# Kernel tuning notes

Hardware: AMD Instinct MI355X
Metric: run time of the kernel (lower is better)

## Reference

```python
import jax, jax.numpy as jnp
import numpy as np

N = 50000
E = 500000
D = 128      # input_nf = output_nf = hidden_nf
EPS = 1e-8
MAX_TRANS = 10.0


def setup_inputs() -> dict:
    key = jax.random.key(0)
    ks = jax.random.split(key, 16)
    s = lambda k, shp: jax.random.normal(k, shp, dtype=jnp.float32) * 0.05
    inp = {
        "h": jax.random.normal(ks[0], (N, D), dtype=jnp.float32),
        "edge_index": jax.random.randint(ks[1], (2, E), 0, N, dtype=jnp.int64),
        "coord": jax.random.normal(ks[2], (N, 3), dtype=jnp.float32),
        # edge_mlp: Linear(2D+1 -> D), SiLU, Linear(D -> D), SiLU
        "We1": s(ks[3], (2 * D + 1, D)), "be1": jnp.zeros((D,), jnp.float32),
        "We2": s(ks[4], (D, D)),         "be2": jnp.zeros((D,), jnp.float32),
        # att_mlp: Linear(D -> 1), Sigmoid
        "Watt": s(ks[5], (D, 1)), "batt": jnp.zeros((1,), jnp.float32),
        # coord_mlp: Linear(D -> D), SiLU, Linear(D -> 1, bias=False, xavier gain=0.001)
        "Wc1": s(ks[6], (D, D)), "bc1": jnp.zeros((D,), jnp.float32),
        "Wc2": s(ks[7], (D, 1)) * 0.001,
        # node_mlp: Linear(2D -> D), SiLU, Linear(D -> D)
        "Wn1": s(ks[8], (2 * D, D)), "bn1": jnp.zeros((D,), jnp.float32),
        "Wn2": s(ks[9], (D, D)),     "bn2": jnp.zeros((D,), jnp.float32),
    }
    return inp


def _segment_mean(data, seg_ids, num_segments):
    tot = jax.ops.segment_sum(data, seg_ids, num_segments=num_segments)
    cnt = jax.ops.segment_sum(jnp.ones_like(data), seg_ids, num_segments=num_segments)
    return tot / jnp.clip(cnt, 1.0, None)


def reference(h, edge_index, coord, We1, be1, We2, be2, Watt, batt,
              Wc1, bc1, Wc2, Wn1, bn1, Wn2, bn2):
    row, col = edge_index[0], edge_index[1]

    # coord2radial (normalize=False)
    coord_diff = coord[row] - coord[col]                      # [E, 3]
    radial = jnp.sum(coord_diff ** 2, axis=1, keepdims=True)  # [E, 1]

    # edge_model with attention
    e_in = jnp.concatenate([h[row], h[col], radial], axis=1)  # [E, 2D+1]
    e = jax.nn.silu(e_in @ We1 + be1)
    edge_feat = jax.nn.silu(e @ We2 + be2)                    # [E, D]
    att = jax.nn.sigmoid(edge_feat @ Watt + batt)             # [E, 1]
    edge_feat = edge_feat * att

    # coord_model (update_coords=True, coords_agg='mean', tanh=False)
    cw = jax.nn.silu(edge_feat @ Wc1 + bc1) @ Wc2             # [E, 1]
    trans = jnp.clip(coord_diff * cw, -MAX_TRANS, MAX_TRANS)  # [E, 3]
    agg_c = jnp.clip(_segment_mean(trans, row, N), -MAX_TRANS, MAX_TRANS)
    coord_out = coord + agg_c

    # node_model (residual=True)
    agg = jax.ops.segment_sum(edge_feat, row, num_segments=N)  # [N, D]
    n_in = jnp.concatenate([h, agg], axis=1)                   # [N, 2D]
    h_out = h + (jax.nn.silu(n_in @ Wn1 + bn1) @ Wn2 + bn2)

    return h_out, coord_out, edge_feat
```

## Files before the change

kernel.cpp:

```cpp
#include <hip/hip_runtime.h>

typedef unsigned short ushort_t;
typedef __attribute__((ext_vector_type(8))) short short8;
typedef __attribute__((ext_vector_type(4))) short short4v;
typedef __attribute__((ext_vector_type(4))) float f32x4;

#define NN 50000
#define EE 500000
#define DD 128
#define MAXT 10.0f

#define MFMA(a,b,c) __builtin_amdgcn_mfma_f32_16x16x32_bf16((a),(b),(c),0,0,0)

__device__ __forceinline__ ushort_t f2bf(float x){
  unsigned u = __float_as_uint(x);
  u += 0x7FFFu + ((u>>16)&1u);
  return (ushort_t)(u>>16);
}
__device__ __forceinline__ float sigm(float x){ return 1.0f/(1.0f+__expf(-x)); }
__device__ __forceinline__ float siluf(float x){ return x*sigm(x); }
__device__ __forceinline__ float clamp10(float x){ return fminf(fmaxf(x,-MAXT),MAXT); }

__global__ void k_prep(const float* __restrict__ We1, const float* __restrict__ We2,
                       const float* __restrict__ Wc1, const float* __restrict__ Wn1,
                       const float* __restrict__ Wn2, ushort_t* __restrict__ wpre)
{
  int idx = blockIdx.x*256 + threadIdx.x;
  if (idx >= 7*16384) return;
  int mat = idx >> 14;
  int loc = idx & 16383;
  int n = loc >> 7;
  int kidx = loc & 127;
  int ko = 16*(kidx&7) + (kidx>>3);
  float v;
  switch(mat){
    case 0: v = We1[kidx*DD + n]; break;
    case 1: v = We1[(128+kidx)*DD + n]; break;
    case 2: v = We2[kidx*DD + n]; break;
    case 3: v = Wc1[ko*DD + n]; break;
    case 4: v = Wn1[kidx*DD + n]; break;
    case 5: v = Wn1[(128+kidx)*DD + n]; break;
    default: v = Wn2[ko*DD + n]; break;
  }
  int byteoff = n*256 + ((kidx*2) ^ ((n&7)<<4));
  *(ushort_t*)((char*)wpre + (size_t)mat*32768 + byteoff) = f2bf(v);
}

__global__ void k_hprep(const float* __restrict__ h, ushort_t* __restrict__ hb)
{
  int i = blockIdx.x*256 + threadIdx.x;
  if (i >= NN*DD/8) return;
  f32x4 x = ((const f32x4*)h)[2*i];
  f32x4 y = ((const f32x4*)h)[2*i+1];
  short8 t;
  #pragma unroll
  for (int j=0;j<4;++j){ t[j]=(short)f2bf(x[j]); t[j+4]=(short)f2bf(y[j]); }
  ((short8*)hb)[i] = t;
}

__global__ void k_zero(int* __restrict__ cnt){
  int i = blockIdx.x*256 + threadIdx.x;
  if (i < NN) cnt[i] = 0;
}
__global__ void k_count(const int* __restrict__ eidx, int* __restrict__ cnt){
  int e = blockIdx.x*256 + threadIdx.x;
  if (e < EE) atomicAdd(&cnt[eidx[e]], 1);
}
#define SCAN_B 196
__global__ void k_bsum(const int* __restrict__ cnt, int* __restrict__ bsum){
  __shared__ int sh[256];
  int t = threadIdx.x;
  int i = blockIdx.x*256 + t;
  sh[t] = (i < NN) ? cnt[i] : 0;
  __syncthreads();
  for (int off=128; off>0; off>>=1){
    if (t < off) sh[t] += sh[t+off];
    __syncthreads();
  }
  if (t==0) bsum[blockIdx.x] = sh[0];
}
__global__ void k_bscan(const int* __restrict__ bsum, int* __restrict__ boff){
  __shared__ int sh[256];
  int t = threadIdx.x;
  sh[t] = (t < SCAN_B) ? bsum[t] : 0;
  __syncthreads();
  for (int off=1; off<256; off<<=1){
    int x = (t>=off) ? sh[t-off] : 0;
    __syncthreads();
    sh[t] += x;
    __syncthreads();
  }
  if (t < SCAN_B) boff[t] = (t>0) ? sh[t-1] : 0;
}
__global__ void k_rscan(const int* __restrict__ cnt, const int* __restrict__ boff,
                        int* __restrict__ rowstart, int* __restrict__ cursor){
  __shared__ int sh[256];
  int t = threadIdx.x;
  int i = blockIdx.x*256 + t;
  int v = (i < NN) ? cnt[i] : 0;
  sh[t] = v;
  __syncthreads();
  for (int off=1; off<256; off<<=1){
    int x = (t>=off) ? sh[t-off] : 0;
    __syncthreads();
    sh[t] += x;
    __syncthreads();
  }
  int excl = sh[t] - v + boff[blockIdx.x];
  if (i < NN){ rowstart[i] = excl; cursor[i] = excl; }
  if (i == 0) rowstart[NN] = EE;
}
__global__ void k_scatter(const int* __restrict__ eidx, int* __restrict__ cursor,
                          int* __restrict__ csr){
  int e = blockIdx.x*256 + threadIdx.x;
  if (e < EE){
    int p = atomicAdd(&cursor[eidx[e]], 1);
    csr[p] = e;
  }
}

__device__ __forceinline__ void stage(const ushort_t* __restrict__ wpre, int mat,
                                      ushort_t* Wbuf, int tid)
{
  const f32x4* src = (const f32x4*)(wpre + (size_t)mat*16384);
  f32x4* dst = (f32x4*)Wbuf;
  #pragma unroll
  for (int i=0;i<4;++i) dst[tid + 512*i] = src[tid + 512*i];
}
__device__ __forceinline__ void zacc(f32x4 acc[2][4]){
  #pragma unroll
  for (int i=0;i<2;++i)
    #pragma unroll
    for (int j=0;j<4;++j) acc[i][j] = (f32x4){0.f,0.f,0.f,0.f};
}
__device__ __forceinline__ void gemm_b16(const short8 af[2][4], const ushort_t* Wbuf,
                                         int cbase, int q, int s, f32x4 acc[2][4])
{
  #pragma unroll
  for (int kc=0;kc<4;++kc){
    const int koff = ((kc*64+q*16) ^ ((s&7)<<4));
    #pragma unroll
    for (int ct=0;ct<4;++ct){
      short8 bf = *(const short8*)((const char*)Wbuf + (cbase+ct*16+s)*256 + koff);
      acc[0][ct] = MFMA(af[0][kc],bf,acc[0][ct]);
      acc[1][ct] = MFMA(af[1][kc],bf,acc[1][ct]);
    }
  }
}
__device__ __forceinline__ void gemm_lds16(const ushort_t* ebuf, const ushort_t* Wbuf,
                                           int mbase, int cbase, int q, int s,
                                           f32x4 acc[2][4])
{
  #pragma unroll
  for (int kc=0;kc<4;++kc){
    const int koff = ((kc*64+q*16) ^ ((s&7)<<4));
    short8 a0 = *(const short8*)((const char*)ebuf + (mbase+s)*256 + koff);
    short8 a1 = *(const short8*)((const char*)ebuf + (mbase+16+s)*256 + koff);
    #pragma unroll
    for (int ct=0;ct<4;++ct){
      short8 bf = *(const short8*)((const char*)Wbuf + (cbase+ct*16+s)*256 + koff);
      acc[0][ct] = MFMA(a0,bf,acc[0][ct]);
      acc[1][ct] = MFMA(a1,bf,acc[1][ct]);
    }
  }
}

__launch_bounds__(512,4)
__global__ void k_pre1(const ushort_t* __restrict__ hb,
                       const ushort_t* __restrict__ wpre,
                       const float* __restrict__ be1,
                       float* __restrict__ H1a, float* __restrict__ H1b)
{
  __shared__ ushort_t Wbuf[16384];
  const int tid = threadIdx.x;
  const int wv = tid>>6, ln = tid&63;
  const int wm = wv&3, wn = wv>>2;
  const int q = ln>>4, s = ln&15;
  const int cbase = wn*64;
  const int n0 = blockIdx.x*128;
  const int mb = wm*32;
  const int nd0 = min(n0 + mb + s,      NN-1);
  const int nd1 = min(n0 + mb + 16 + s, NN-1);

  f32x4 acc[2][4];
  short8 af[2][4];
  zacc(acc);
  #pragma unroll
  for (int kc=0;kc<4;++kc){
    af[0][kc] = *(const short8*)(hb + (size_t)nd0*DD + kc*32 + q*8);
    af[1][kc] = *(const short8*)(hb + (size_t)nd1*DD + kc*32 + q*8);
  }
  stage(wpre, 0, Wbuf, tid);
  __syncthreads();
  gemm_b16(af, Wbuf, cbase, q, s, acc);
  {
    float bb[4];
    #pragma unroll
    for (int ct=0;ct<4;++ct) bb[ct]=be1[cbase+16*ct+s];
    #pragma unroll
    for (int mt=0;mt<2;++mt)
      #pragma unroll
      for (int r=0;r<4;++r){
        int n = n0 + mb + mt*16 + q*4 + r;
        if (n < NN){
          float* op = H1a + (size_t)n*DD + cbase + s;
          #pragma unroll
          for (int ct=0;ct<4;++ct) op[16*ct] = acc[mt][ct][r] + bb[ct];
        }
      }
  }
  zacc(acc);
  __syncthreads();
  stage(wpre, 1, Wbuf, tid);
  __syncthreads();
  gemm_b16(af, Wbuf, cbase, q, s, acc);
  {
    #pragma unroll
    for (int mt=0;mt<2;++mt)
      #pragma unroll
      for (int r=0;r<4;++r){
        int n = n0 + mb + mt*16 + q*4 + r;
        if (n < NN){
          float* op = H1b + (size_t)n*DD + cbase + s;
          #pragma unroll
          for (int ct=0;ct<4;++ct) op[16*ct] = acc[mt][ct][r];
        }
      }
  }
}

__launch_bounds__(512,4)
__global__ void k_edge(const float* __restrict__ H1a,
                       const float* __restrict__ H1b,
                       const int* __restrict__ eidx,
                       const int* __restrict__ csr,
                       const float* __restrict__ coord,
                       const float* __restrict__ We1,
                       const float* __restrict__ be2,
                       const float* __restrict__ Watt,
                       const float* __restrict__ batt,
                       const float* __restrict__ bc1,
                       const float* __restrict__ Wc2,
                       const ushort_t* __restrict__ wpre,
                       float* __restrict__ ef_out,
                       float* __restrict__ trans)
{
  __shared__ ushort_t Wbuf[16384];
  __shared__ ushort_t ebuf[16384];
  __shared__ float dscr[128][2];
  const int tid = threadIdx.x;
  const int wv = tid>>6, ln = tid&63;
  const int wm = wv&3, wn = wv>>2;
  const int q = ln>>4, s = ln&15;
  const int cbase = wn*64;
  const int eb0 = blockIdx.x*128;
  const int mb = wm*32;
  const int* rowI = eidx;
  const int* colI = eidx + EE;

  const int jg = eb0 + mb + (ln&31);
  const int og = csr[min(jg, EE-1)];
  const int rg = rowI[og], cg = colI[og];
  const float cdx = coord[rg*3+0]-coord[cg*3+0];
  const float cdy = coord[rg*3+1]-coord[cg*3+1];
  const float cdz = coord[rg*3+2]-coord[cg*3+2];

  const int o0 = csr[min(eb0+mb+s,    EE-1)];
  const int o1 = csr[min(eb0+mb+16+s, EE-1)];
  const int r0 = rowI[o0], c0 = colI[o0];
  const int r1 = rowI[o1], c1 = colI[o1];
  float rad[2];
  { float dx=coord[r0*3+0]-coord[c0*3+0], dy=coord[r0*3+1]-coord[c0*3+1],
          dz=coord[r0*3+2]-coord[c0*3+2];
    rad[0]=dx*dx+dy*dy+dz*dz; }
  { float dx=coord[r1*3+0]-coord[c1*3+0], dy=coord[r1*3+1]-coord[c1*3+1],
          dz=coord[r1*3+2]-coord[c1*3+2];
    rad[1]=dx*dx+dy*dy+dz*dz; }

  stage(wpre, 2, Wbuf, tid);

  #pragma unroll
  for (int mt=0; mt<2; ++mt){
    const int nR = mt ? r1 : r0, nC = mt ? c1 : c0;
    const float rd = rad[mt];
    const int m = mb + mt*16 + s;
    #pragma unroll
    for (int gi=0; gi<2; ++gi){
      const int g = wn*8 + q*2 + gi;
      const f32x4* pa = (const f32x4*)(H1a + (size_t)nR*DD + g*8);
      const f32x4* pb = (const f32x4*)(H1b + (size_t)nC*DD + g*8);
      const f32x4* pw = (const f32x4*)(We1 + 256*DD + g*8);
      f32x4 a0=pa[0], a1=pa[1], bv0=pb[0], bv1=pb[1], w0=pw[0], w1=pw[1];
      short8 pk;
      #pragma unroll
      for (int t=0;t<4;++t){
        pk[t]   = (short)f2bf(siluf(a0[t]+bv0[t]+rd*w0[t]));
        pk[t+4] = (short)f2bf(siluf(a1[t]+bv1[t]+rd*w1[t]));
      }
      *(short8*)((char*)ebuf + m*256 + ((g*16) ^ ((m&7)<<4))) = pk;
    }
  }

  f32x4 acc[2][4];
  zacc(acc);
  __syncthreads();

  gemm_lds16(ebuf, Wbuf, mb, cbase, q, s, acc);
  {
    float wa[4], bb[4];
    #pragma unroll
    for (int ct=0;ct<4;++ct){ wa[ct]=Watt[cbase+16*ct+s]; bb[ct]=be2[cbase+16*ct+s]; }
    #pragma unroll
    for (int mt=0;mt<2;++mt){
      #pragma unroll
      for (int r=0;r<4;++r){
        float p = 0.f;
        #pragma unroll
        for (int ct=0;ct<4;++ct){
          float v = siluf(acc[mt][ct][r] + bb[ct]);
          acc[mt][ct][r] = v;
          p += v*wa[ct];
        }
        p += __shfl_xor(p,1); p += __shfl_xor(p,2);
        p += __shfl_xor(p,4); p += __shfl_xor(p,8);
        if (s==0) dscr[mb + mt*16 + q*4 + r][wn] = p;
      }
    }
  }
  __syncthreads();
  stage(wpre, 3, Wbuf, tid);
  {
    const float bat = batt[0];
    #pragma unroll
    for (int mt=0;mt<2;++mt){
      #pragma unroll
      for (int r=0;r<4;++r){
        int m = mb + mt*16 + q*4 + r;
        float att = sigm(dscr[m][0] + dscr[m][1] + bat);
        short4v pk;
        #pragma unroll
        for (int ct=0;ct<4;++ct){
          acc[mt][ct][r] *= att;
          pk[ct]=(short)f2bf(acc[mt][ct][r]);
        }
        *(short4v*)((char*)ebuf + m*256 + ((16*s+8*wn) ^ ((m&7)<<4))) = pk;
        int js = eb0 + m;
        if (js < EE){
          float* rp = ef_out + (size_t)csr[js]*DD + cbase + s;
          #pragma unroll
          for (int ct=0;ct<4;++ct) rp[16*ct] = acc[mt][ct][r];
        }
      }
    }
  }
  zacc(acc);
  __syncthreads();

  gemm_lds16(ebuf, Wbuf, mb, cbase, q, s, acc);
  {
    float wc[4], bb[4];
    #pragma unroll
    for (int ct=0;ct<4;++ct){ wc[ct]=Wc2[cbase+16*ct+s]; bb[ct]=bc1[cbase+16*ct+s]; }
    #pragma unroll
    for (int mt=0;mt<2;++mt){
      #pragma unroll
      for (int r=0;r<4;++r){
        float p = 0.f;
        #pragma unroll
        for (int ct=0;ct<4;++ct) p += siluf(acc[mt][ct][r]+bb[ct])*wc[ct];
        p += __shfl_xor(p,1); p += __shfl_xor(p,2);
        p += __shfl_xor(p,4); p += __shfl_xor(p,8);
        if (s==0) dscr[mb + mt*16 + q*4 + r][wn] = p;
      }
    }
  }
  __syncthreads();
  if (wn==0 && ln<32 && jg < EE){
    float p = dscr[mb+ln][0] + dscr[mb+ln][1];
    trans[(size_t)jg*3+0] = clamp10(cdx*p);
    trans[(size_t)jg*3+1] = clamp10(cdy*p);
    trans[(size_t)jg*3+2] = clamp10(cdz*p);
  }
}

__launch_bounds__(256)
__global__ void k_agg(const float* __restrict__ ef,
                      const float* __restrict__ trans,
                      const int* __restrict__ rowstart,
                      const int* __restrict__ csr,
                      const float* __restrict__ coord,
                      ushort_t* __restrict__ aggb,
                      float* __restrict__ coord_out)
{
  const int wv = threadIdx.x>>6, ln = threadIdx.x&63;
  const int n = blockIdx.x*4 + wv;
  if (n >= NN) return;
  const int rs = rowstart[n], re = rowstart[n+1];
  const int deg = re - rs;
  const int half = ln>>5, l4 = (ln&31)*4;
  float a0=0,a1=0,a2=0,a3=0;
  for (int j=half; j<deg; j+=2){
    const float* p = ef + (size_t)csr[rs+j]*DD + l4;
    f32x4 v = *(const f32x4*)p;
    a0+=v[0]; a1+=v[1]; a2+=v[2]; a3+=v[3];
  }
  a0 += __shfl_xor(a0,32); a1 += __shfl_xor(a1,32);
  a2 += __shfl_xor(a2,32); a3 += __shfl_xor(a3,32);
  if (half==0){
    short4v o = { (short)f2bf(a0),(short)f2bf(a1),(short)f2bf(a2),(short)f2bf(a3) };
    *(short4v*)(aggb + (size_t)n*DD + l4) = o;
  }
  float tx=0,ty=0,tz=0;
  for (int j=ln;j<deg;j+=64){
    const float* t = trans + (size_t)(rs+j)*3;
    tx+=t[0]; ty+=t[1]; tz+=t[2];
  }
  #pragma unroll
  for (int m=1;m<64;m<<=1){
    tx+=__shfl_xor(tx,m); ty+=__shfl_xor(ty,m); tz+=__shfl_xor(tz,m);
  }
  if (ln==0){
    const float inv = 1.0f/(float)max(deg,1);
    coord_out[(size_t)n*3+0] = coord[(size_t)n*3+0] + clamp10(tx*inv);
    coord_out[(size_t)n*3+1] = coord[(size_t)n*3+1] + clamp10(ty*inv);
    coord_out[(size_t)n*3+2] = coord[(size_t)n*3+2] + clamp10(tz*inv);
  }
}

__launch_bounds__(512,4)
__global__ void k_node(const float* __restrict__ h,
                       const ushort_t* __restrict__ hb,
                       const ushort_t* __restrict__ aggb,
                       const ushort_t* __restrict__ wpre,
                       const float* __restrict__ bn1,
                       const float* __restrict__ bn2,
                       float* __restrict__ hout)
{
  __shared__ ushort_t Wbuf[16384];
  __shared__ ushort_t ubuf[16384];
  const int tid = threadIdx.x;
  const int wv = tid>>6, ln = tid&63;
  const int wm = wv&3, wn = wv>>2;
  const int q = ln>>4, s = ln&15;
  const int cbase = wn*64;
  const int n0 = blockIdx.x*128;
  const int mb = wm*32;
  const int nd0 = min(n0 + mb + s,      NN-1);
  const int nd1 = min(n0 + mb + 16 + s, NN-1);

  f32x4 acc[2][4];
  short8 af[2][4];
  zacc(acc);

  #pragma unroll
  for (int kc=0;kc<4;++kc){
    af[0][kc] = *(const short8*)(hb + (size_t)nd0*DD + kc*32 + q*8);
    af[1][kc] = *(const short8*)(hb + (size_t)nd1*DD + kc*32 + q*8);
  }
  stage(wpre, 4, Wbuf, tid);
  __syncthreads();
  gemm_b16(af, Wbuf, cbase, q, s, acc);

  #pragma unroll
  for (int kc=0;kc<4;++kc){
    af[0][kc] = *(const short8*)(aggb + (size_t)nd0*DD + kc*32 + q*8);
    af[1][kc] = *(const short8*)(aggb + (size_t)nd1*DD + kc*32 + q*8);
  }
  __syncthreads();
  stage(wpre, 5, Wbuf, tid);
  __syncthreads();
  gemm_b16(af, Wbuf, cbase, q, s, acc);

  {
    float bb[4];
    #pragma unroll
    for (int ct=0;ct<4;++ct) bb[ct]=bn1[cbase+16*ct+s];
    #pragma unroll
    for (int mt=0;mt<2;++mt){
      #pragma unroll
      for (int r=0;r<4;++r){
        int m = mb + mt*16 + q*4 + r;
        short4v pk;
        #pragma unroll
        for (int ct=0;ct<4;++ct) pk[ct]=(short)f2bf(siluf(acc[mt][ct][r]+bb[ct]));
        *(short4v*)((char*)ubuf + m*256 + ((16*s+8*wn) ^ ((m&7)<<4))) = pk;
      }
    }
  }
  zacc(acc);
  __syncthreads();
  stage(wpre, 6, Wbuf, tid);
  __syncthreads();

  gemm_lds16(ubuf, Wbuf, mb, cbase, q, s, acc);

  {
    float bb[4];
    #pragma unroll
    for (int ct=0;ct<4;++ct) bb[ct]=bn2[cbase+16*ct+s];
    #pragma unroll
    for (int mt=0;mt<2;++mt){
      #pragma unroll
      for (int r=0;r<4;++r){
        int n = n0 + mb + mt*16 + q*4 + r;
        if (n < NN){
          const float* hp = h + (size_t)n*DD + cbase + s;
          float* op = hout + (size_t)n*DD + cbase + s;
          #pragma unroll
          for (int ct=0;ct<4;++ct) op[16*ct] = hp[16*ct] + acc[mt][ct][r] + bb[ct];
        }
      }
    }
  }
}

extern "C" void kernel_launch(void* const* d_in, const int* in_sizes, int n_in,
                              void* d_out, int out_size, void* d_ws, size_t ws_size,
                              hipStream_t stream)
{
  const float* h    = (const float*)d_in[0];
  const int*   eidx = (const int*)  d_in[1];
  const float* coord= (const float*)d_in[2];
  const float* We1  = (const float*)d_in[3];
  const float* be1  = (const float*)d_in[4];
  const float* We2  = (const float*)d_in[5];
  const float* be2  = (const float*)d_in[6];
  const float* Watt = (const float*)d_in[7];
  const float* batt = (const float*)d_in[8];
  const float* Wc1  = (const float*)d_in[9];
  const float* bc1  = (const float*)d_in[10];
  const float* Wc2  = (const float*)d_in[11];
  const float* Wn1  = (const float*)d_in[12];
  const float* bn1  = (const float*)d_in[13];
  const float* Wn2  = (const float*)d_in[14];
  const float* bn2  = (const float*)d_in[15];

  float* hout     = (float*)d_out;
  float* coordout = hout + (size_t)NN*DD;
  float* efout    = coordout + (size_t)NN*3;

  char* ws = (char*)d_ws;
  float*    trans = (float*)(ws);
  ushort_t* aggb  = (ushort_t*)(ws + 6000000);
  ushort_t* hb    = (ushort_t*)(ws + 18800000);
  int*   cnt     = (int*)  (ws + 31600000);
  int*   cursor  = (int*)  (ws + 31800000);
  int*   rowstart= (int*)  (ws + 32000000);
  int*   csr     = (int*)  (ws + 32200064);
  ushort_t* wpre = (ushort_t*)(ws + 34200064);
  float* H1a     = (float*)(ws + 34429440);
  float* H1b     = (float*)(ws + 60029440);
  int*   bsum    = csr;
  int*   boff    = csr + 256;

  k_prep   <<<448, 256, 0, stream>>>(We1, We2, Wc1, Wn1, Wn2, wpre);
  k_hprep  <<<3125,256, 0, stream>>>(h, hb);
  k_zero   <<<196, 256, 0, stream>>>(cnt);
  k_count  <<<1954,256, 0, stream>>>(eidx, cnt);
  k_bsum   <<<196, 256, 0, stream>>>(cnt, bsum);
  k_bscan  <<<1,   256, 0, stream>>>(bsum, boff);
  k_rscan  <<<196, 256, 0, stream>>>(cnt, boff, rowstart, cursor);
  k_scatter<<<1954,256, 0, stream>>>(eidx, cursor, csr);
  k_pre1   <<<391, 512, 0, stream>>>(hb, wpre, be1, H1a, H1b);
  k_edge   <<<3907,512, 0, stream>>>(H1a, H1b, eidx, csr, coord, We1, be2, Watt,
                                     batt, bc1, Wc2, wpre, efout, trans);
  k_agg    <<<12500,256,0, stream>>>(efout, trans, rowstart, csr, coord, aggb, coordout);
  k_node   <<<391, 512, 0, stream>>>(h, hb, aggb, wpre, bn1, bn2, hout);
}
```

Before: 699.2 us.

## Fuse segment aggregation into edge kernel via sorted-run atomics, drop hprep and agg kernels

The edge kernel now reduces edge features into per-node sums itself. It stages the scaled edge features in shared memory, runs a run-length sum over the CSR-sorted rows, and issues float atomics to a global fp32 agg buffer. Coordinate translations are atomically added into tsum, and the coord mean is finished in k_node. The separate bf16 h conversion kernel and the k_agg gather kernel are removed, with h converted on load inside k_pre1 and k_node, and the zero-fill kernel is replaced with memsets. This saves a full re-read of edge_feat and a kernel launch. In exchange it adds atomic contention, memset traffic for a 25.6MB agg buffer, and nondeterministic summation order.

```diff
diff --git a/kernel.cpp b/kernel.cpp
--- a/kernel.cpp
+++ b/kernel.cpp
@@ -20,6 +20,15 @@
 __device__ __forceinline__ float sigm(float x){ return 1.0f/(1.0f+__expf(-x)); }
 __device__ __forceinline__ float siluf(float x){ return x*sigm(x); }
 __device__ __forceinline__ float clamp10(float x){ return fminf(fmaxf(x,-MAXT),MAXT); }
+
+__device__ __forceinline__ short8 ldcvt(const float* p){
+  f32x4 x = *(const f32x4*)p;
+  f32x4 y = *(const f32x4*)(p+4);
+  short8 t;
+  #pragma unroll
+  for (int j=0;j<4;++j){ t[j]=(short)f2bf(x[j]); t[j+4]=(short)f2bf(y[j]); }
+  return t;
+}
 
 __global__ void k_prep(const float* __restrict__ We1, const float* __restrict__ We2,
                        const float* __restrict__ Wc1, const float* __restrict__ Wn1,
@@ -46,22 +55,6 @@
   *(ushort_t*)((char*)wpre + (size_t)mat*32768 + byteoff) = f2bf(v);
 }
 
-__global__ void k_hprep(const float* __restrict__ h, ushort_t* __restrict__ hb)
-{
-  int i = blockIdx.x*256 + threadIdx.x;
-  if (i >= NN*DD/8) return;
-  f32x4 x = ((const f32x4*)h)[2*i];
-  f32x4 y = ((const f32x4*)h)[2*i+1];
-  short8 t;
-  #pragma unroll
-  for (int j=0;j<4;++j){ t[j]=(short)f2bf(x[j]); t[j+4]=(short)f2bf(y[j]); }
-  ((short8*)hb)[i] = t;
-}
-
-__global__ void k_zero(int* __restrict__ cnt){
-  int i = blockIdx.x*256 + threadIdx.x;
-  if (i < NN) cnt[i] = 0;
-}
 __global__ void k_count(const int* __restrict__ eidx, int* __restrict__ cnt){
   int e = blockIdx.x*256 + threadIdx.x;
   if (e < EE) atomicAdd(&cnt[eidx[e]], 1);
@@ -166,7 +159,7 @@
 }
 
 __launch_bounds__(512,4)
-__global__ void k_pre1(const ushort_t* __restrict__ hb,
+__global__ void k_pre1(const float* __restrict__ h,
                        const ushort_t* __restrict__ wpre,
                        const float* __restrict__ be1,
                        float* __restrict__ H1a, float* __restrict__ H1b)
@@ -187,8 +180,8 @@
   zacc(acc);
   #pragma unroll
   for (int kc=0;kc<4;++kc){
-    af[0][kc] = *(const short8*)(hb + (size_t)nd0*DD + kc*32 + q*8);
-    af[1][kc] = *(const short8*)(hb + (size_t)nd1*DD + kc*32 + q*8);
+    af[0][kc] = ldcvt(h + (size_t)nd0*DD + kc*32 + q*8);
+    af[1][kc] = ldcvt(h + (size_t)nd1*DD + kc*32 + q*8);
   }
   stage(wpre, 0, Wbuf, tid);
   __syncthreads();
@@ -243,11 +236,16 @@
                        const float* __restrict__ Wc2,
                        const ushort_t* __restrict__ wpre,
                        float* __restrict__ ef_out,
-                       float* __restrict__ trans)
-{
-  __shared__ ushort_t Wbuf[16384];
-  __shared__ ushort_t ebuf[16384];
-  __shared__ float dscr[128][2];
+                       float* __restrict__ agg,
+                       float* __restrict__ tsum)
+{
+  __shared__ __align__(16) char smem[67072];
+  ushort_t* Wbuf = (ushort_t*)smem;
+  ushort_t* ebuf = (ushort_t*)(smem + 32768);
+  float (*dscr)[2] = (float(*)[2])(smem + 65536);
+  int* rowLDS = (int*)(smem + 66560);
+  float* aggLDS = (float*)smem;
+
   const int tid = threadIdx.x;
   const int wv = tid>>6, ln = tid&63;
   const int wm = wv&3, wn = wv>>2;
@@ -279,25 +277,33 @@
 
   stage(wpre, 2, Wbuf, tid);
 
-  #pragma unroll
-  for (int mt=0; mt<2; ++mt){
-    const int nR = mt ? r1 : r0, nC = mt ? c1 : c0;
-    const float rd = rad[mt];
-    const int m = mb + mt*16 + s;
+  {
+    f32x4 w0[2], w1[2];
     #pragma unroll
     for (int gi=0; gi<2; ++gi){
       const int g = wn*8 + q*2 + gi;
-      const f32x4* pa = (const f32x4*)(H1a + (size_t)nR*DD + g*8);
-      const f32x4* pb = (const f32x4*)(H1b + (size_t)nC*DD + g*8);
       const f32x4* pw = (const f32x4*)(We1 + 256*DD + g*8);
-      f32x4 a0=pa[0], a1=pa[1], bv0=pb[0], bv1=pb[1], w0=pw[0], w1=pw[1];
-      short8 pk;
-      #pragma unroll
-      for (int t=0;t<4;++t){
-        pk[t]   = (short)f2bf(siluf(a0[t]+bv0[t]+rd*w0[t]));
-        pk[t+4] = (short)f2bf(siluf(a1[t]+bv1[t]+rd*w1[t]));
-      }
-      *(short8*)((char*)ebuf + m*256 + ((g*16) ^ ((m&7)<<4))) = pk;
+      w0[gi]=pw[0]; w1[gi]=pw[1];
+    }
+    #pragma unroll
+    for (int mt=0; mt<2; ++mt){
+      const int nR = mt ? r1 : r0, nC = mt ? c1 : c0;
+      const float rd = rad[mt];
+      const int m = mb + mt*16 + s;
+      #pragma unroll
+      for (int gi=0; gi<2; ++gi){
+        const int g = wn*8 + q*2 + gi;
+        const f32x4* pa = (const f32x4*)(H1a + (size_t)nR*DD + g*8);
+        const f32x4* pb = (const f32x4*)(H1b + (size_t)nC*DD + g*8);
+        f32x4 a0=pa[0], a1=pa[1], bv0=pb[0], bv1=pb[1];
+        short8 pk;
+        #pragma unroll
+        for (int t=0;t<4;++t){
+          pk[t]   = (short)f2bf(siluf(a0[t]+bv0[t]+rd*w0[gi][t]));
+          pk[t+4] = (short)f2bf(siluf(a1[t]+bv1[t]+rd*w1[gi][t]));
+        }
+        *(short8*)((char*)ebuf + m*256 + ((g*16) ^ ((m&7)<<4))) = pk;
+      }
     }
   }
 
@@ -353,10 +359,11 @@
       }
     }
   }
-  zacc(acc);
-  __syncthreads();
-
-  gemm_lds16(ebuf, Wbuf, mb, cbase, q, s, acc);
+  __syncthreads();
+
+  f32x4 acc2[2][4];
+  zacc(acc2);
+  gemm_lds16(ebuf, Wbuf, mb, cbase, q, s, acc2);
   {
     float wc[4], bb[4];
     #pragma unroll
@@ -367,7 +374,7 @@
       for (int r=0;r<4;++r){
         float p = 0.f;
         #pragma unroll
-        for (int ct=0;ct<4;++ct) p += siluf(acc[mt][ct][r]+bb[ct])*wc[ct];
+        for (int ct=0;ct<4;++ct) p += siluf(acc2[mt][ct][r]+bb[ct])*wc[ct];
         p += __shfl_xor(p,1); p += __shfl_xor(p,2);
         p += __shfl_xor(p,4); p += __shfl_xor(p,8);
         if (s==0) dscr[mb + mt*16 + q*4 + r][wn] = p;
@@ -375,66 +382,66 @@
     }
   }
   __syncthreads();
-  if (wn==0 && ln<32 && jg < EE){
-    float p = dscr[mb+ln][0] + dscr[mb+ln][1];
-    trans[(size_t)jg*3+0] = clamp10(cdx*p);
-    trans[(size_t)jg*3+1] = clamp10(cdy*p);
-    trans[(size_t)jg*3+2] = clamp10(cdz*p);
-  }
-}
-
-__launch_bounds__(256)
-__global__ void k_agg(const float* __restrict__ ef,
-                      const float* __restrict__ trans,
-                      const int* __restrict__ rowstart,
-                      const int* __restrict__ csr,
-                      const float* __restrict__ coord,
-                      ushort_t* __restrict__ aggb,
-                      float* __restrict__ coord_out)
-{
-  const int wv = threadIdx.x>>6, ln = threadIdx.x&63;
-  const int n = blockIdx.x*4 + wv;
-  if (n >= NN) return;
-  const int rs = rowstart[n], re = rowstart[n+1];
-  const int deg = re - rs;
-  const int half = ln>>5, l4 = (ln&31)*4;
-  float a0=0,a1=0,a2=0,a3=0;
-  for (int j=half; j<deg; j+=2){
-    const float* p = ef + (size_t)csr[rs+j]*DD + l4;
-    f32x4 v = *(const f32x4*)p;
-    a0+=v[0]; a1+=v[1]; a2+=v[2]; a3+=v[3];
-  }
-  a0 += __shfl_xor(a0,32); a1 += __shfl_xor(a1,32);
-  a2 += __shfl_xor(a2,32); a3 += __shfl_xor(a3,32);
-  if (half==0){
-    short4v o = { (short)f2bf(a0),(short)f2bf(a1),(short)f2bf(a2),(short)f2bf(a3) };
-    *(short4v*)(aggb + (size_t)n*DD + l4) = o;
-  }
-  float tx=0,ty=0,tz=0;
-  for (int j=ln;j<deg;j+=64){
-    const float* t = trans + (size_t)(rs+j)*3;
-    tx+=t[0]; ty+=t[1]; tz+=t[2];
-  }
-  #pragma unroll
-  for (int m=1;m<64;m<<=1){
-    tx+=__shfl_xor(tx,m); ty+=__shfl_xor(ty,m); tz+=__shfl_xor(tz,m);
-  }
-  if (ln==0){
-    const float inv = 1.0f/(float)max(deg,1);
-    coord_out[(size_t)n*3+0] = coord[(size_t)n*3+0] + clamp10(tx*inv);
-    coord_out[(size_t)n*3+1] = coord[(size_t)n*3+1] + clamp10(ty*inv);
-    coord_out[(size_t)n*3+2] = coord[(size_t)n*3+2] + clamp10(tz*inv);
+
+  if (wn==0 && ln<32){
+    rowLDS[mb+ln] = rg;
+    if (jg < EE){
+      float p = dscr[mb+ln][0] + dscr[mb+ln][1];
+      atomicAdd(&tsum[(size_t)rg*3+0], clamp10(cdx*p));
+      atomicAdd(&tsum[(size_t)rg*3+1], clamp10(cdy*p));
+      atomicAdd(&tsum[(size_t)rg*3+2], clamp10(cdz*p));
+    }
+  }
+
+  #pragma unroll
+  for (int mt=0;mt<2;++mt){
+    #pragma unroll
+    for (int r=0;r<4;++r){
+      const int m = mb + mt*16 + q*4 + r;
+      char* base = (char*)aggLDS + m*512;
+      #pragma unroll
+      for (int ct=0;ct<4;++ct){
+        const int c = cbase + 16*ct + s;
+        *(float*)(base + ((c*4) ^ ((m&7)<<4))) = acc[mt][ct][r];
+      }
+    }
+  }
+  __syncthreads();
+
+  {
+    const int c = tid & 127;
+    const int sub = tid >> 7;
+    const int mmax = min(128, EE - eb0);
+    const int m0 = sub*32;
+    if (m0 < mmax){
+      const int mend = min(m0+32, mmax);
+      int currow = rowLDS[m0];
+      float sum = 0.f;
+      for (int m=m0; m<mend; ++m){
+        int rr = rowLDS[m];
+        float v = *(const float*)((const char*)aggLDS + m*512 + ((c*4) ^ ((m&7)<<4)));
+        if (rr != currow){
+          atomicAdd(&agg[(size_t)currow*DD + c], sum);
+          sum = 0.f; currow = rr;
+        }
+        sum += v;
+      }
+      atomicAdd(&agg[(size_t)currow*DD + c], sum);
+    }
   }
 }
 
 __launch_bounds__(512,4)
 __global__ void k_node(const float* __restrict__ h,
-                       const ushort_t* __restrict__ hb,
-                       const ushort_t* __restrict__ aggb,
+                       const float* __restrict__ agg,
+                       const float* __restrict__ tsum,
+                       const int* __restrict__ rowstart,
+                       const float* __restrict__ coord,
                        const ushort_t* __restrict__ wpre,
                        const float* __restrict__ bn1,
                        const float* __restrict__ bn2,
-                       float* __restrict__ hout)
+                       float* __restrict__ hout,
+                       float* __restrict__ coord_out)
 {
   __shared__ ushort_t Wbuf[16384];
   __shared__ ushort_t ubuf[16384];
@@ -448,14 +455,26 @@
   const int nd0 = min(n0 + mb + s,      NN-1);
   const int nd1 = min(n0 + mb + 16 + s, NN-1);
 
+  if (tid < 128){
+    int n = n0 + tid;
+    if (n < NN){
+      int dg = rowstart[n+1] - rowstart[n];
+      float inv = 1.0f/(float)max(dg,1);
+      #pragma unroll
+      for (int d=0; d<3; ++d)
+        coord_out[(size_t)n*3+d] = coord[(size_t)n*3+d]
+                                 + clamp10(tsum[(size_t)n*3+d]*inv);
+    }
+  }
+
   f32x4 acc[2][4];
   short8 af[2][4];
   zacc(acc);
 
   #pragma unroll
   for (int kc=0;kc<4;++kc){
-    af[0][kc] = *(const short8*)(hb + (size_t)nd0*DD + kc*32 + q*8);
-    af[1][kc] = *(const short8*)(hb + (size_t)nd1*DD + kc*32 + q*8);
+    af[0][kc] = ldcvt(h + (size_t)nd0*DD + kc*32 + q*8);
+    af[1][kc] = ldcvt(h + (size_t)nd1*DD + kc*32 + q*8);
   }
   stage(wpre, 4, Wbuf, tid);
   __syncthreads();
@@ -463,8 +482,8 @@
 
   #pragma unroll
   for (int kc=0;kc<4;++kc){
-    af[0][kc] = *(const short8*)(aggb + (size_t)nd0*DD + kc*32 + q*8);
-    af[1][kc] = *(const short8*)(aggb + (size_t)nd1*DD + kc*32 + q*8);
+    af[0][kc] = ldcvt(agg + (size_t)nd0*DD + kc*32 + q*8);
+    af[1][kc] = ldcvt(agg + (size_t)nd1*DD + kc*32 + q*8);
   }
   __syncthreads();
   stage(wpre, 5, Wbuf, tid);
@@ -540,30 +559,30 @@
   float* efout    = coordout + (size_t)NN*3;
 
   char* ws = (char*)d_ws;
-  float*    trans = (float*)(ws);
-  ushort_t* aggb  = (ushort_t*)(ws + 6000000);
-  ushort_t* hb    = (ushort_t*)(ws + 18800000);
-  int*   cnt     = (int*)  (ws + 31600000);
-  int*   cursor  = (int*)  (ws + 31800000);
-  int*   rowstart= (int*)  (ws + 32000000);
-  int*   csr     = (int*)  (ws + 32200064);
-  ushort_t* wpre = (ushort_t*)(ws + 34200064);
-  float* H1a     = (float*)(ws + 34429440);
-  float* H1b     = (float*)(ws + 60029440);
-  int*   bsum    = csr;
-  int*   boff    = csr + 256;
-
+  float* tsum     = (float*)(ws);
+  float* agg      = (float*)(ws + 600000);
+  int*   cnt      = (int*)  (ws + 26200000);
+  int*   cursor   = (int*)  (ws + 26400000);
+  int*   rowstart = (int*)  (ws + 26600000);
+  int*   csr      = (int*)  (ws + 26800064);
+  ushort_t* wpre  = (ushort_t*)(ws + 28800064);
+  float* H1a      = (float*)(ws + 29029440);
+  float* H1b      = (float*)(ws + 54629440);
+  int*   bsum     = csr;
+  int*   boff     = csr + 256;
+
+  hipMemsetAsync(tsum, 0,   600000, stream);
+  hipMemsetAsync(agg,  0, 25600000, stream);
+  hipMemsetAsync(cnt,  0,   200000, stream);
   k_prep   <<<448, 256, 0, stream>>>(We1, We2, Wc1, Wn1, Wn2, wpre);
-  k_hprep  <<<3125,256, 0, stream>>>(h, hb);
-  k_zero   <<<196, 256, 0, stream>>>(cnt);
   k_count  <<<1954,256, 0, stream>>>(eidx, cnt);
   k_bsum   <<<196, 256, 0, stream>>>(cnt, bsum);
   k_bscan  <<<1,   256, 0, stream>>>(bsum, boff);
   k_rscan  <<<196, 256, 0, stream>>>(cnt, boff, rowstart, cursor);
   k_scatter<<<1954,256, 0, stream>>>(eidx, cursor, csr);
-  k_pre1   <<<391, 512, 0, stream>>>(hb, wpre, be1, H1a, H1b);
+  k_pre1   <<<391, 512, 0, stream>>>(h, wpre, be1, H1a, H1b);
   k_edge   <<<3907,512, 0, stream>>>(H1a, H1b, eidx, csr, coord, We1, be2, Watt,
-                                     batt, bc1, Wc2, wpre, efout, trans);
-  k_agg    <<<12500,256,0, stream>>>(efout, trans, rowstart, csr, coord, aggb, coordout);
-  k_node   <<<391, 512, 0, stream>>>(h, hb, aggb, wpre, bn1, bn2, hout);
-}
+                                     batt, bc1, Wc2, wpre, efout, agg, tsum);
+  k_node   <<<391, 512, 0, stream>>>(h, agg, tsum, rowstart, coord, wpre,
+                                     bn1, bn2, hout, coordout);
+}
```

New measurement: 701.0 us. Within noise of the previous version (+0.3%).

## Store H1 projections in bf16, process edges in original order, drop h prep kernel

Applied to the files above, without the earlier changes.

The per-node first-layer projections H1a/H1b are now written and gathered as bf16 instead of fp32, halving the bytes read per edge in the edge kernel. The edge kernel now walks edges in their original order rather than CSR-sorted order, so edge_feat and trans writes become contiguous, and the aggregation kernel reads trans through the CSR permutation instead. The separate h-to-bf16 kernel is removed by converting h on load in the GEMM kernels, and the counter-zeroing kernel is replaced by a memset. Trade-offs are extra rounding of the H1 intermediates, and the loss of row-sorted locality for the H1a gathers in the edge kernel.

```diff
diff --git a/kernel.cpp b/kernel.cpp
--- a/kernel.cpp
+++ b/kernel.cpp
@@ -17,9 +17,21 @@
   u += 0x7FFFu + ((u>>16)&1u);
   return (ushort_t)(u>>16);
 }
+__device__ __forceinline__ float bf2f(ushort_t u){
+  return __uint_as_float(((unsigned)u)<<16);
+}
 __device__ __forceinline__ float sigm(float x){ return 1.0f/(1.0f+__expf(-x)); }
 __device__ __forceinline__ float siluf(float x){ return x*sigm(x); }
 __device__ __forceinline__ float clamp10(float x){ return fminf(fmaxf(x,-MAXT),MAXT); }
+
+__device__ __forceinline__ short8 ldcvt(const float* p){
+  f32x4 x = *(const f32x4*)p;
+  f32x4 y = *(const f32x4*)(p+4);
+  short8 t;
+  #pragma unroll
+  for (int j=0;j<4;++j){ t[j]=(short)f2bf(x[j]); t[j+4]=(short)f2bf(y[j]); }
+  return t;
+}
 
 __global__ void k_prep(const float* __restrict__ We1, const float* __restrict__ We2,
                        const float* __restrict__ Wc1, const float* __restrict__ Wn1,
@@ -46,22 +58,6 @@
   *(ushort_t*)((char*)wpre + (size_t)mat*32768 + byteoff) = f2bf(v);
 }
 
-__global__ void k_hprep(const float* __restrict__ h, ushort_t* __restrict__ hb)
-{
-  int i = blockIdx.x*256 + threadIdx.x;
-  if (i >= NN*DD/8) return;
-  f32x4 x = ((const f32x4*)h)[2*i];
-  f32x4 y = ((const f32x4*)h)[2*i+1];
-  short8 t;
-  #pragma unroll
-  for (int j=0;j<4;++j){ t[j]=(short)f2bf(x[j]); t[j+4]=(short)f2bf(y[j]); }
-  ((short8*)hb)[i] = t;
-}
-
-__global__ void k_zero(int* __restrict__ cnt){
-  int i = blockIdx.x*256 + threadIdx.x;
-  if (i < NN) cnt[i] = 0;
-}
 __global__ void k_count(const int* __restrict__ eidx, int* __restrict__ cnt){
   int e = blockIdx.x*256 + threadIdx.x;
   if (e < EE) atomicAdd(&cnt[eidx[e]], 1);
@@ -166,10 +162,10 @@
 }
 
 __launch_bounds__(512,4)
-__global__ void k_pre1(const ushort_t* __restrict__ hb,
+__global__ void k_pre1(const float* __restrict__ h,
                        const ushort_t* __restrict__ wpre,
                        const float* __restrict__ be1,
-                       float* __restrict__ H1a, float* __restrict__ H1b)
+                       ushort_t* __restrict__ H1a, ushort_t* __restrict__ H1b)
 {
   __shared__ ushort_t Wbuf[16384];
   const int tid = threadIdx.x;
@@ -187,8 +183,8 @@
   zacc(acc);
   #pragma unroll
   for (int kc=0;kc<4;++kc){
-    af[0][kc] = *(const short8*)(hb + (size_t)nd0*DD + kc*32 + q*8);
-    af[1][kc] = *(const short8*)(hb + (size_t)nd1*DD + kc*32 + q*8);
+    af[0][kc] = ldcvt(h + (size_t)nd0*DD + kc*32 + q*8);
+    af[1][kc] = ldcvt(h + (size_t)nd1*DD + kc*32 + q*8);
   }
   stage(wpre, 0, Wbuf, tid);
   __syncthreads();
@@ -203,9 +199,9 @@
       for (int r=0;r<4;++r){
         int n = n0 + mb + mt*16 + q*4 + r;
         if (n < NN){
-          float* op = H1a + (size_t)n*DD + cbase + s;
+          ushort_t* op = H1a + (size_t)n*DD + cbase + s;
           #pragma unroll
-          for (int ct=0;ct<4;++ct) op[16*ct] = acc[mt][ct][r] + bb[ct];
+          for (int ct=0;ct<4;++ct) op[16*ct] = f2bf(acc[mt][ct][r] + bb[ct]);
         }
       }
   }
@@ -221,19 +217,18 @@
       for (int r=0;r<4;++r){
         int n = n0 + mb + mt*16 + q*4 + r;
         if (n < NN){
-          float* op = H1b + (size_t)n*DD + cbase + s;
+          ushort_t* op = H1b + (size_t)n*DD + cbase + s;
           #pragma unroll
-          for (int ct=0;ct<4;++ct) op[16*ct] = acc[mt][ct][r];
+          for (int ct=0;ct<4;++ct) op[16*ct] = f2bf(acc[mt][ct][r]);
         }
       }
   }
 }
 
 __launch_bounds__(512,4)
-__global__ void k_edge(const float* __restrict__ H1a,
-                       const float* __restrict__ H1b,
+__global__ void k_edge(const ushort_t* __restrict__ H1a,
+                       const ushort_t* __restrict__ H1b,
                        const int* __restrict__ eidx,
-                       const int* __restrict__ csr,
                        const float* __restrict__ coord,
                        const float* __restrict__ We1,
                        const float* __restrict__ be2,
@@ -253,22 +248,22 @@
   const int wm = wv&3, wn = wv>>2;
   const int q = ln>>4, s = ln&15;
   const int cbase = wn*64;
-  const int eb0 = blockIdx.x*128;
+  const int we0 = blockIdx.x*128;
   const int mb = wm*32;
   const int* rowI = eidx;
   const int* colI = eidx + EE;
 
-  const int jg = eb0 + mb + (ln&31);
-  const int og = csr[min(jg, EE-1)];
-  const int rg = rowI[og], cg = colI[og];
+  const int jg = we0 + mb + (ln&31);
+  const int jgc = min(jg, EE-1);
+  const int rg = rowI[jgc], cg = colI[jgc];
   const float cdx = coord[rg*3+0]-coord[cg*3+0];
   const float cdy = coord[rg*3+1]-coord[cg*3+1];
   const float cdz = coord[rg*3+2]-coord[cg*3+2];
 
-  const int o0 = csr[min(eb0+mb+s,    EE-1)];
-  const int o1 = csr[min(eb0+mb+16+s, EE-1)];
-  const int r0 = rowI[o0], c0 = colI[o0];
-  const int r1 = rowI[o1], c1 = colI[o1];
+  const int e0 = min(we0+mb+s,    EE-1);
+  const int e1 = min(we0+mb+16+s, EE-1);
+  const int r0 = rowI[e0], c0 = colI[e0];
+  const int r1 = rowI[e1], c1 = colI[e1];
   float rad[2];
   { float dx=coord[r0*3+0]-coord[c0*3+0], dy=coord[r0*3+1]-coord[c0*3+1],
           dz=coord[r0*3+2]-coord[c0*3+2];
@@ -279,25 +274,34 @@
 
   stage(wpre, 2, Wbuf, tid);
 
-  #pragma unroll
-  for (int mt=0; mt<2; ++mt){
-    const int nR = mt ? r1 : r0, nC = mt ? c1 : c0;
-    const float rd = rad[mt];
-    const int m = mb + mt*16 + s;
+  {
+    float w[2][8];
     #pragma unroll
     for (int gi=0; gi<2; ++gi){
       const int g = wn*8 + q*2 + gi;
-      const f32x4* pa = (const f32x4*)(H1a + (size_t)nR*DD + g*8);
-      const f32x4* pb = (const f32x4*)(H1b + (size_t)nC*DD + g*8);
       const f32x4* pw = (const f32x4*)(We1 + 256*DD + g*8);
-      f32x4 a0=pa[0], a1=pa[1], bv0=pb[0], bv1=pb[1], w0=pw[0], w1=pw[1];
-      short8 pk;
-      #pragma unroll
-      for (int t=0;t<4;++t){
-        pk[t]   = (short)f2bf(siluf(a0[t]+bv0[t]+rd*w0[t]));
-        pk[t+4] = (short)f2bf(siluf(a1[t]+bv1[t]+rd*w1[t]));
-      }
-      *(short8*)((char*)ebuf + m*256 + ((g*16) ^ ((m&7)<<4))) = pk;
+      f32x4 w0=pw[0], w1=pw[1];
+      #pragma unroll
+      for (int t=0;t<4;++t){ w[gi][t]=w0[t]; w[gi][t+4]=w1[t]; }
+    }
+    #pragma unroll
+    for (int mt=0; mt<2; ++mt){
+      const int nR = mt ? r1 : r0, nC = mt ? c1 : c0;
+      const float rd = rad[mt];
+      const int m = mb + mt*16 + s;
+      #pragma unroll
+      for (int gi=0; gi<2; ++gi){
+        const int g = wn*8 + q*2 + gi;
+        short8 sa = *(const short8*)(H1a + (size_t)nR*DD + g*8);
+        short8 sb = *(const short8*)(H1b + (size_t)nC*DD + g*8);
+        short8 pk;
+        #pragma unroll
+        for (int t=0;t<8;++t){
+          float e = bf2f((ushort_t)sa[t]) + bf2f((ushort_t)sb[t]) + rd*w[gi][t];
+          pk[t] = (short)f2bf(siluf(e));
+        }
+        *(short8*)((char*)ebuf + m*256 + ((g*16) ^ ((m&7)<<4))) = pk;
+      }
     }
   }
 
@@ -344,9 +348,9 @@
           pk[ct]=(short)f2bf(acc[mt][ct][r]);
         }
         *(short4v*)((char*)ebuf + m*256 + ((16*s+8*wn) ^ ((m&7)<<4))) = pk;
-        int js = eb0 + m;
-        if (js < EE){
-          float* rp = ef_out + (size_t)csr[js]*DD + cbase + s;
+        int e = we0 + m;
+        if (e < EE){
+          float* rp = ef_out + (size_t)e*DD + cbase + s;
           #pragma unroll
           for (int ct=0;ct<4;++ct) rp[16*ct] = acc[mt][ct][r];
         }
@@ -412,7 +416,7 @@
   }
   float tx=0,ty=0,tz=0;
   for (int j=ln;j<deg;j+=64){
-    const float* t = trans + (size_t)(rs+j)*3;
+    const float* t = trans + (size_t)csr[rs+j]*3;
     tx+=t[0]; ty+=t[1]; tz+=t[2];
   }
   #pragma unroll
@@ -429,7 +433,6 @@
 
 __launch_bounds__(512,4)
 __global__ void k_node(const float* __restrict__ h,
-                       const ushort_t* __restrict__ hb,
                        const ushort_t* __restrict__ aggb,
                        const ushort_t* __restrict__ wpre,
                        const float* __restrict__ bn1,
@@ -454,8 +457,8 @@
 
   #pragma unroll
   for (int kc=0;kc<4;++kc){
-    af[0][kc] = *(const short8*)(hb + (size_t)nd0*DD + kc*32 + q*8);
-    af[1][kc] = *(const short8*)(hb + (size_t)nd1*DD + kc*32 + q*8);
+    af[0][kc] = ldcvt(h + (size_t)nd0*DD + kc*32 + q*8);
+    af[1][kc] = ldcvt(h + (size_t)nd1*DD + kc*32 + q*8);
   }
   stage(wpre, 4, Wbuf, tid);
   __syncthreads();
@@ -542,28 +545,26 @@
   char* ws = (char*)d_ws;
   float*    trans = (float*)(ws);
   ushort_t* aggb  = (ushort_t*)(ws + 6000000);
-  ushort_t* hb    = (ushort_t*)(ws + 18800000);
-  int*   cnt     = (int*)  (ws + 31600000);
-  int*   cursor  = (int*)  (ws + 31800000);
-  int*   rowstart= (int*)  (ws + 32000000);
-  int*   csr     = (int*)  (ws + 32200064);
-  ushort_t* wpre = (ushort_t*)(ws + 34200064);
-  float* H1a     = (float*)(ws + 34429440);
-  float* H1b     = (float*)(ws + 60029440);
-  int*   bsum    = csr;
-  int*   boff    = csr + 256;
-
+  int*   cnt      = (int*)  (ws + 18800000);
+  int*   cursor   = (int*)  (ws + 19000000);
+  int*   rowstart = (int*)  (ws + 19200000);
+  int*   csr      = (int*)  (ws + 19400064);
+  ushort_t* wpre  = (ushort_t*)(ws + 21400064);
+  ushort_t* H1a   = (ushort_t*)(ws + 21629440);
+  ushort_t* H1b   = (ushort_t*)(ws + 34429440);
+  int*   bsum     = csr;
+  int*   boff     = csr + 256;
+
+  hipMemsetAsync(cnt, 0, 200000, stream);
   k_prep   <<<448, 256, 0, stream>>>(We1, We2, Wc1, Wn1, Wn2, wpre);
-  k_hprep  <<<3125,256, 0, stream>>>(h, hb);
-  k_zero   <<<196, 256, 0, stream>>>(cnt);
   k_count  <<<1954,256, 0, stream>>>(eidx, cnt);
   k_bsum   <<<196, 256, 0, stream>>>(cnt, bsum);
   k_bscan  <<<1,   256, 0, stream>>>(bsum, boff);
   k_rscan  <<<196, 256, 0, stream>>>(cnt, boff, rowstart, cursor);
   k_scatter<<<1954,256, 0, stream>>>(eidx, cursor, csr);
-  k_pre1   <<<391, 512, 0, stream>>>(hb, wpre, be1, H1a, H1b);
-  k_edge   <<<3907,512, 0, stream>>>(H1a, H1b, eidx, csr, coord, We1, be2, Watt,
+  k_pre1   <<<391, 512, 0, stream>>>(h, wpre, be1, H1a, H1b);
+  k_edge   <<<3907,512, 0, stream>>>(H1a, H1b, eidx, coord, We1, be2, Watt,
                                      batt, bc1, Wc2, wpre, efout, trans);
   k_agg    <<<12500,256,0, stream>>>(efout, trans, rowstart, csr, coord, aggb, coordout);
-  k_node   <<<391, 512, 0, stream>>>(h, hb, aggb, wpre, bn1, bn2, hout);
-}
+  k_node   <<<391, 512, 0, stream>>>(h, aggb, wpre, bn1, bn2, hout);
+}
```

Measured after the change: 627.2 us. 10.3% less time.
